# Kernel tuning notes

Hardware: AMD Instinct MI355X
Metric: run time of the kernel (lower is better)

## Reference

```python
import jax, jax.numpy as jnp
import numpy as np
from jax import lax

K = 3          # dcn kernel size
KK = K * K     # 9 taps
PAD = 1


def _conv(x, w, b, pad):
    y = lax.conv_general_dilated(
        x, w, window_strides=(1, 1), padding=[(pad, pad), (pad, pad)],
        dimension_numbers=("NCHW", "OIHW", "NCHW"))
    return y + b[None, :, None, None]


def _bilinear_gather(x, py, px):
    """Zero-padded bilinear sampling.
    x: [B,C,Hin,Win]; py,px: [B,KK,H,W] float sample coords.
    returns [B,C,KK,H,W]."""
    B, C, Hin, Win = x.shape
    y0 = jnp.floor(py)
    x0 = jnp.floor(px)
    ly = py - y0   # frac weights
    lx = px - x0
    xf = x.reshape(B, C, Hin * Win)

    def corner(yc, xc, w):
        valid = (yc >= 0) & (yc <= Hin - 1) & (xc >= 0) & (xc <= Win - 1)
        yi = jnp.clip(yc, 0, Hin - 1).astype(jnp.int32)
        xi = jnp.clip(xc, 0, Win - 1).astype(jnp.int32)
        idx = yi * Win + xi                              # [B,KK,H,W]
        vals = jax.vmap(lambda f, i: jnp.take(f, i, axis=1))(xf, idx)  # [B,C,KK,H,W]
        return vals * (w * valid.astype(x.dtype))[:, None]

    out = corner(y0,     x0,     (1 - ly) * (1 - lx))
    out = out + corner(y0,     x0 + 1, (1 - ly) * lx)
    out = out + corner(y0 + 1, x0,     ly * (1 - lx))
    out = out + corner(y0 + 1, x0 + 1, ly * lx)
    return out


def _forward(x, conv1_w, conv1_b, off_w, off_b, dcn_w, dcn_b):
    # features: Conv2d(1,3,3,s1,p1) + ReLU + MaxPool(3,2)
    h = jax.nn.relu(_conv(x, conv1_w, conv1_b, pad=1))
    h = lax.reduce_window(h, -jnp.inf, lax.max,
                          window_dimensions=(1, 1, 3, 3),
                          window_strides=(1, 1, 2, 2), padding="VALID")
    B, C, H, W = h.shape

    # DCNv2: conv_offset_mask -> (dy, dx, sigmoid mask)
    om = _conv(h, off_w, off_b, pad=PAD)          # [B, 3*KK, H, W]
    dy = om[:, :KK]
    dx = om[:, KK:2 * KK]
    mask = jax.nn.sigmoid(om[:, 2 * KK:])         # [B, KK, H, W]

    # base sampling grid (stride 1, pad 1, dilation 1)
    ky = (jnp.arange(KK) // K).astype(h.dtype)    # kernel row of each tap
    kx = (jnp.arange(KK) % K).astype(h.dtype)
    hh = jnp.arange(H, dtype=h.dtype)
    ww = jnp.arange(W, dtype=h.dtype)
    py = hh[None, None, :, None] - PAD + ky[None, :, None, None] + dy
    px = ww[None, None, None, :] - PAD + kx[None, :, None, None] + dx

    sampled = _bilinear_gather(h, py, px)          # [B,C,KK,H,W]
    sampled = sampled * mask[:, None]              # modulation
    out = jnp.einsum("bckhw,ock->bohw", sampled,
                     dcn_w.reshape(dcn_w.shape[0], C, KK))
    return out + dcn_b[None, :, None, None]


def setup_inputs() -> dict:
    key = jax.random.key(0)
    ks = jax.random.split(key, 7)
    x = jax.random.normal(ks[0], (32, 1, 512, 512), dtype=jnp.float32)
    conv1_w = jax.random.normal(ks[1], (3, 1, 3, 3), dtype=jnp.float32) * 0.5
    conv1_b = jnp.zeros((3,), dtype=jnp.float32)
    # offset/mask conv: 3*KK = 27 output channels; small init so offsets are modest
    off_w = jax.random.normal(ks[2], (3 * KK, 3, 3, 3), dtype=jnp.float32) * 0.01
    off_b = jax.random.normal(ks[3], (3 * KK,), dtype=jnp.float32) * 0.01
    dcn_w = jax.random.normal(ks[4], (3, 3, 3, 3), dtype=jnp.float32) * 0.1
    dcn_b = jnp.zeros((3,), dtype=jnp.float32)
    return {"x": x, "conv1_w": conv1_w, "conv1_b": conv1_b,
            "off_w": off_w, "off_b": off_b, "dcn_w": dcn_w, "dcn_b": dcn_b}


def reference(x, conv1_w, conv1_b, off_w, off_b, dcn_w, dcn_b):
    return _forward(x, conv1_w, conv1_b, off_w, off_b, dcn_w, dcn_b)
```

## Files before the change

kernel.cpp:

```cpp
#include <hip/hip_runtime.h>
#include <math.h>

#define B_  32
#define H0  512
#define W0  512
#define Hh  255
#define Wh  255
#define HP  259

typedef __attribute__((ext_vector_type(8))) short    bf16x8;
typedef __attribute__((ext_vector_type(4))) float    f32x4;
typedef __attribute__((ext_vector_type(4))) unsigned int u32x4;

static __device__ __forceinline__ unsigned int f2bf(float f) {
    unsigned int u = __float_as_uint(f);
    return (u + 0x7FFFu + ((u >> 16) & 1u)) >> 16;
}
static __device__ __forceinline__ float bflo(unsigned int u) { return __uint_as_float(u << 16); }
static __device__ __forceinline__ float bfhi(unsigned int u) { return __uint_as_float(u & 0xFFFF0000u); }

__global__ __launch_bounds__(256) void conv_pool_kernel(
    const float* __restrict__ x,
    const float* __restrict__ w,
    const float* __restrict__ bias,
    uint2* __restrict__ hp)
{
    const int b = blockIdx.z;
    const int tx = threadIdx.x, ty = threadIdx.y;
    const int tid = ty * 16 + tx;

    if (blockIdx.y == 16) {
        uint2* hpb = hp + b * (HP * HP);
        const int gid = blockIdx.x * 256 + tid;
        if (gid < 2072) {
            int r, c;
            if (gid < 1036) {
                int rr = gid / 259; c = gid - rr * 259;
                r = rr + (rr >= 2 ? 255 : 0);
            } else {
                int u = gid - 1036;
                int cc = u / 259; r = u - cc * 259;
                c = cc + (cc >= 2 ? 255 : 0);
            }
            hpb[r * HP + c] = make_uint2(0u, 0u);
        }
        return;
    }

    __shared__ float sx[35][36];
    __shared__ float sc[33 * 100];
    const int i0 = blockIdx.y * 16;
    const int j0 = blockIdx.x * 16;

    const float* xb = x + b * (H0 * W0);
    for (int t = tid; t < 35 * 35; t += 256) {
        int r = t / 35, c = t - r * 35;
        int gr = 2 * i0 - 1 + r;
        int gc = 2 * j0 - 1 + c;
        float v = 0.f;
        if ((unsigned)gr < (unsigned)H0 && (unsigned)gc < (unsigned)W0) v = xb[gr * W0 + gc];
        sx[r][c] = v;
    }
    __syncthreads();

    float w0[9], w1[9], w2[9];
#pragma unroll
    for (int t = 0; t < 9; ++t) { w0[t] = w[t]; w1[t] = w[9 + t]; w2[t] = w[18 + t]; }
    const float b0 = bias[0], b1 = bias[1], b2 = bias[2];

    for (int t = tid; t < 33 * 33; t += 256) {
        int r = t / 33, c = t - r * 33;
        float s0 = b0, s1 = b1, s2 = b2;
#pragma unroll
        for (int ky = 0; ky < 3; ++ky) {
#pragma unroll
            for (int kx = 0; kx < 3; ++kx) {
                float v = sx[r + ky][c + kx];
                s0 = fmaf(w0[ky * 3 + kx], v, s0);
                s1 = fmaf(w1[ky * 3 + kx], v, s1);
                s2 = fmaf(w2[ky * 3 + kx], v, s2);
            }
        }
        float* p = &sc[r * 100 + c * 3];
        p[0] = s0; p[1] = s1; p[2] = s2;
    }
    __syncthreads();

    const int i = i0 + ty, j = j0 + tx;
    if (i >= Hh || j >= Wh) return;

    const float* r0 = &sc[(2 * ty + 0) * 100 + (2 * tx) * 3];
    const float* r1 = &sc[(2 * ty + 1) * 100 + (2 * tx) * 3];
    const float* r2 = &sc[(2 * ty + 2) * 100 + (2 * tx) * 3];
#define MAX3_(a, bq, cq) fmaxf(fmaxf((a), (bq)), (cq))
    float m0 = MAX3_(MAX3_(r0[0], r0[3], r0[6]), MAX3_(r1[0], r1[3], r1[6]), MAX3_(r2[0], r2[3], r2[6]));
    float m1 = MAX3_(MAX3_(r0[1], r0[4], r0[7]), MAX3_(r1[1], r1[4], r1[7]), MAX3_(r2[1], r2[4], r2[7]));
    float m2 = MAX3_(MAX3_(r0[2], r0[5], r0[8]), MAX3_(r1[2], r1[5], r1[8]), MAX3_(r2[2], r2[5], r2[8]));
    m0 = fmaxf(m0, 0.f); m1 = fmaxf(m1, 0.f); m2 = fmaxf(m2, 0.f);

    uint2 v;
    v.x = f2bf(m0) | (f2bf(m1) << 16);
    v.y = f2bf(m2);
    hp[(b * HP + i + 2) * HP + (j + 2)] = v;
}

__global__ __launch_bounds__(256, 5) void dcn_kernel(
    const uint2* __restrict__ hp,
    const float* __restrict__ off_w,
    const float* __restrict__ off_b,
    const float* __restrict__ dcn_w,
    const float* __restrict__ dcn_b,
    float* __restrict__ out)
{
    __shared__ __align__(16) char smem[18432];

    const int y   = blockIdx.x;
    const int b   = blockIdx.y;
    const int tid = threadIdx.x;
    const int x   = tid;

    const uint2* hb = hp + b * (HP * HP);

    {
        unsigned short* Bm = (unsigned short*)(smem + 16384);
        for (int idx = tid; idx < 1024; idx += 256) {
            int n = idx >> 5, k = idx & 31;
            float v = 0.f;
            if (n < 27) { if (k < 27) v = off_w[n * 27 + k]; else if (k == 27) v = off_b[n]; }
            Bm[n * 32 + k] = (unsigned short)f2bf(v);
        }
    }

    unsigned int L[9], Hv[9];
#pragma unroll
    for (int ky = 0; ky < 3; ++ky) {
        const unsigned int rbase = (unsigned int)(y + 1 + ky) * HP + (unsigned int)(x + 1);
#pragma unroll
        for (int kx = 0; kx < 3; ++kx) {
            uint2 v = hb[rbase + kx];
            L[ky * 3 + kx]  = v.x;
            Hv[ky * 3 + kx] = v.y;
        }
    }

    {
        unsigned int T[16];
        T[0]  = (L[0] & 0xFFFFu) | (L[1] << 16);
        T[1]  = (L[2] & 0xFFFFu) | (L[3] << 16);
        T[2]  = (L[4] & 0xFFFFu) | (L[5] << 16);
        T[3]  = (L[6] & 0xFFFFu) | (L[7] << 16);
        T[4]  = (L[8] & 0xFFFFu) | (L[0] & 0xFFFF0000u);
        T[5]  = (L[1] >> 16) | (L[2] & 0xFFFF0000u);
        T[6]  = (L[3] >> 16) | (L[4] & 0xFFFF0000u);
        T[7]  = (L[5] >> 16) | (L[6] & 0xFFFF0000u);
        T[8]  = (L[7] >> 16) | (L[8] & 0xFFFF0000u);
        T[9]  = (Hv[0] & 0xFFFFu) | (Hv[1] << 16);
        T[10] = (Hv[2] & 0xFFFFu) | (Hv[3] << 16);
        T[11] = (Hv[4] & 0xFFFFu) | (Hv[5] << 16);
        T[12] = (Hv[6] & 0xFFFFu) | (Hv[7] << 16);
        T[13] = (Hv[8] & 0xFFFFu) | 0x3F800000u;
        T[14] = 0u;
        T[15] = 0u;
#pragma unroll
        for (int c4 = 0; c4 < 4; ++c4) {
            u32x4 v = { T[c4 * 4 + 0], T[c4 * 4 + 1], T[c4 * 4 + 2], T[c4 * 4 + 3] };
            *(u32x4*)(smem + (c4 * 256 + tid) * 16) = v;
        }
    }
    __syncthreads();

    {
        const int wave = tid >> 6, lane = tid & 63;
        const int lrow = lane & 15, lchunk = lane >> 4;
        const short* As = (const short*)smem;
        const short* Bs = (const short*)(smem + 16384);

        bf16x8 afr[4];
#pragma unroll
        for (int m = 0; m < 4; ++m)
            afr[m] = *(const bf16x8*)(As + (lchunk * 256 + wave * 64 + m * 16 + lrow) * 8);
        bf16x8 bfr[2];
#pragma unroll
        for (int nt = 0; nt < 2; ++nt)
            bfr[nt] = *(const bf16x8*)(Bs + ((nt * 16 + lrow) * 32 + lchunk * 8));

        f32x4 acc[4][2];
#pragma unroll
        for (int m = 0; m < 4; ++m)
#pragma unroll
            for (int nt = 0; nt < 2; ++nt) {
                f32x4 z = {0.f, 0.f, 0.f, 0.f};
                acc[m][nt] = __builtin_amdgcn_mfma_f32_16x16x32_bf16(bfr[nt], afr[m], z, 0, 0, 0);
            }
        __syncthreads();

#pragma unroll
        for (int m = 0; m < 4; ++m)
#pragma unroll
            for (int nt = 0; nt < 2; ++nt) {
                const int n0  = nt * 16 + lchunk * 4;
                const int pxw = wave * 64 + m * 16 + lrow;
                unsigned int p0 = (__float_as_uint(acc[m][nt][0]) >> 16) |
                                  (__float_as_uint(acc[m][nt][1]) & 0xFFFF0000u);
                unsigned int p1 = (__float_as_uint(acc[m][nt][2]) >> 16) |
                                  (__float_as_uint(acc[m][nt][3]) & 0xFFFF0000u);
                unsigned int* q = (unsigned int*)(smem + pxw * 68 + n0 * 2);
                q[0] = p0;
                q[1] = p1;
            }
    }
    __syncthreads();

    unsigned int o2[14];
    {
        const unsigned int* omp = (const unsigned int*)(smem + x * 68);
#pragma unroll
        for (int j = 0; j < 14; ++j) o2[j] = omp[j];
    }
#define OM_(n) (((n) & 1) ? bfhi(o2[(n) >> 1]) : bflo(o2[(n) >> 1]))

    float outv0 = dcn_b[0], outv1 = dcn_b[1], outv2 = dcn_b[2];
    const float yf = (float)y, xf = (float)x;

#pragma unroll
    for (int k = 0; k < 9; ++k) {
        const float dy  = OM_(k);
        const float dxx = OM_(9 + k);
        const float zm  = OM_(18 + k);
        const float msk = __builtin_amdgcn_rcpf(1.f + __expf(-zm));

        const float py = yf + (float)(k / 3 - 1) + dy;
        const float px = xf + (float)(k % 3 - 1) + dxx;

        const float y0f = floorf(py), x0f = floorf(px);
        const float ly = py - y0f, lx = px - x0f;
        int iy = (int)y0f + 2, ix = (int)x0f + 2;
        iy = min(max(iy, 0), 257);
        ix = min(max(ix, 0), 257);

        const unsigned int idx = (unsigned int)iy * HP + (unsigned int)ix;
        u32x4 ua, ub;
        __builtin_memcpy(&ua, hb + idx, 16);
        __builtin_memcpy(&ub, hb + idx + HP, 16);

        const float my1 = ly * msk;
        const float my0 = msk - my1;
        const float lx1 = 1.f - lx;
        const float w00 = my0 * lx1, w01 = my0 * lx;
        const float w10 = my1 * lx1, w11 = my1 * lx;

        const float s0 = w00 * bflo(ua.x) + w01 * bflo(ua.z) + w10 * bflo(ub.x) + w11 * bflo(ub.z);
        const float s1 = w00 * bfhi(ua.x) + w01 * bfhi(ua.z) + w10 * bfhi(ub.x) + w11 * bfhi(ub.z);
        const float s2 = w00 * bflo(ua.y) + w01 * bflo(ua.w) + w10 * bflo(ub.y) + w11 * bflo(ub.w);

        outv0 = fmaf(dcn_w[0 * 27 + 0 * 9 + k], s0, outv0);
        outv0 = fmaf(dcn_w[0 * 27 + 1 * 9 + k], s1, outv0);
        outv0 = fmaf(dcn_w[0 * 27 + 2 * 9 + k], s2, outv0);
        outv1 = fmaf(dcn_w[1 * 27 + 0 * 9 + k], s0, outv1);
        outv1 = fmaf(dcn_w[1 * 27 + 1 * 9 + k], s1, outv1);
        outv1 = fmaf(dcn_w[1 * 27 + 2 * 9 + k], s2, outv1);
        outv2 = fmaf(dcn_w[2 * 27 + 0 * 9 + k], s0, outv2);
        outv2 = fmaf(dcn_w[2 * 27 + 1 * 9 + k], s1, outv2);
        outv2 = fmaf(dcn_w[2 * 27 + 2 * 9 + k], s2, outv2);
    }

    if (x < Wh) {
        const int hwsz = Hh * Wh;
        const int o = (b * 3) * hwsz + y * Wh + x;
        out[o]            = outv0;
        out[o + hwsz]     = outv1;
        out[o + 2 * hwsz] = outv2;
    }
}

extern "C" void kernel_launch(void* const* d_in, const int* in_sizes, int n_in,
                              void* d_out, int out_size, void* d_ws, size_t ws_size,
                              hipStream_t stream) {
    const float* x       = (const float*)d_in[0];
    const float* conv1_w = (const float*)d_in[1];
    const float* conv1_b = (const float*)d_in[2];
    const float* off_w   = (const float*)d_in[3];
    const float* off_b   = (const float*)d_in[4];
    const float* dcn_w   = (const float*)d_in[5];
    const float* dcn_b   = (const float*)d_in[6];
    float* out = (float*)d_out;
    uint2* hp  = (uint2*)d_ws;

    conv_pool_kernel<<<dim3(16, 17, B_), dim3(16, 16), 0, stream>>>(x, conv1_w, conv1_b, hp);
    dcn_kernel<<<dim3(Hh, B_), 256, 0, stream>>>(hp, off_w, off_b, dcn_w, dcn_b, out);
}
```

Baseline: 69.87 us.

## Switch intermediate storage and MFMA from bf16 to fp16 with packed half2 bilinear math

The pooled feature map and offset-conv weights are now stored as fp16 instead of bf16, and the offset MFMA uses the f16 variant. The bilinear corner blend becomes packed half2 FMAs instead of scalar fp32 FMAs with bf16 unpacking. The 3x3 neighbourhood load is also widened to one 16-byte load plus one 8-byte load per row. This aims to cut VALU instruction count in the gather loop, at the cost of lower accumulation precision in fp16 and possible overflow or accuracy risk.

```diff
diff --git a/kernel.cpp b/kernel.cpp
--- a/kernel.cpp
+++ b/kernel.cpp
@@ -1,4 +1,5 @@
 #include <hip/hip_runtime.h>
+#include <hip/hip_fp16.h>
 #include <math.h>
 
 #define B_  32
@@ -8,16 +9,16 @@
 #define Wh  255
 #define HP  259
 
-typedef __attribute__((ext_vector_type(8))) short    bf16x8;
+typedef __attribute__((ext_vector_type(8))) _Float16 f16x8;
 typedef __attribute__((ext_vector_type(4))) float    f32x4;
 typedef __attribute__((ext_vector_type(4))) unsigned int u32x4;
 
-static __device__ __forceinline__ unsigned int f2bf(float f) {
-    unsigned int u = __float_as_uint(f);
-    return (u + 0x7FFFu + ((u >> 16) & 1u)) >> 16;
-}
-static __device__ __forceinline__ float bflo(unsigned int u) { return __uint_as_float(u << 16); }
-static __device__ __forceinline__ float bfhi(unsigned int u) { return __uint_as_float(u & 0xFFFF0000u); }
+static __device__ __forceinline__ __half2 u2h2(unsigned int u) {
+    __half2 h; __builtin_memcpy(&h, &u, 4); return h;
+}
+static __device__ __forceinline__ unsigned int h2u(__half2 h) {
+    unsigned int u; __builtin_memcpy(&u, &h, 4); return u;
+}
 
 __global__ __launch_bounds__(256) void conv_pool_kernel(
     const float* __restrict__ x,
@@ -99,8 +100,8 @@
     m0 = fmaxf(m0, 0.f); m1 = fmaxf(m1, 0.f); m2 = fmaxf(m2, 0.f);
 
     uint2 v;
-    v.x = f2bf(m0) | (f2bf(m1) << 16);
-    v.y = f2bf(m2);
+    v.x = h2u(__floats2half2_rn(m0, m1));
+    v.y = (unsigned int)__half_as_ushort(__float2half_rn(m2));
     hp[(b * HP + i + 2) * HP + (j + 2)] = v;
 }
 
@@ -127,7 +128,7 @@
             int n = idx >> 5, k = idx & 31;
             float v = 0.f;
             if (n < 27) { if (k < 27) v = off_w[n * 27 + k]; else if (k == 27) v = off_b[n]; }
-            Bm[n * 32 + k] = (unsigned short)f2bf(v);
+            Bm[n * 32 + k] = __half_as_ushort(__float2half_rn(v));
         }
     }
 
@@ -135,12 +136,12 @@
 #pragma unroll
     for (int ky = 0; ky < 3; ++ky) {
         const unsigned int rbase = (unsigned int)(y + 1 + ky) * HP + (unsigned int)(x + 1);
-#pragma unroll
-        for (int kx = 0; kx < 3; ++kx) {
-            uint2 v = hb[rbase + kx];
-            L[ky * 3 + kx]  = v.x;
-            Hv[ky * 3 + kx] = v.y;
-        }
+        u32x4 r01;
+        __builtin_memcpy(&r01, hb + rbase, 16);
+        uint2 r2 = hb[rbase + 2];
+        L[ky * 3 + 0]  = r01.x;  Hv[ky * 3 + 0] = r01.y;
+        L[ky * 3 + 1]  = r01.z;  Hv[ky * 3 + 1] = r01.w;
+        L[ky * 3 + 2]  = r2.x;   Hv[ky * 3 + 2] = r2.y;
     }
 
     {
@@ -158,7 +159,7 @@
         T[10] = (Hv[2] & 0xFFFFu) | (Hv[3] << 16);
         T[11] = (Hv[4] & 0xFFFFu) | (Hv[5] << 16);
         T[12] = (Hv[6] & 0xFFFFu) | (Hv[7] << 16);
-        T[13] = (Hv[8] & 0xFFFFu) | 0x3F800000u;
+        T[13] = (Hv[8] & 0xFFFFu) | 0x3C000000u;
         T[14] = 0u;
         T[15] = 0u;
 #pragma unroll
@@ -172,17 +173,17 @@
     {
         const int wave = tid >> 6, lane = tid & 63;
         const int lrow = lane & 15, lchunk = lane >> 4;
-        const short* As = (const short*)smem;
-        const short* Bs = (const short*)(smem + 16384);
-
-        bf16x8 afr[4];
+        const _Float16* As = (const _Float16*)smem;
+        const _Float16* Bs = (const _Float16*)(smem + 16384);
+
+        f16x8 afr[4];
 #pragma unroll
         for (int m = 0; m < 4; ++m)
-            afr[m] = *(const bf16x8*)(As + (lchunk * 256 + wave * 64 + m * 16 + lrow) * 8);
-        bf16x8 bfr[2];
+            afr[m] = *(const f16x8*)(As + (lchunk * 256 + wave * 64 + m * 16 + lrow) * 8);
+        f16x8 bfr[2];
 #pragma unroll
         for (int nt = 0; nt < 2; ++nt)
-            bfr[nt] = *(const bf16x8*)(Bs + ((nt * 16 + lrow) * 32 + lchunk * 8));
+            bfr[nt] = *(const f16x8*)(Bs + ((nt * 16 + lrow) * 32 + lchunk * 8));
 
         f32x4 acc[4][2];
 #pragma unroll
@@ -190,7 +191,7 @@
 #pragma unroll
             for (int nt = 0; nt < 2; ++nt) {
                 f32x4 z = {0.f, 0.f, 0.f, 0.f};
-                acc[m][nt] = __builtin_amdgcn_mfma_f32_16x16x32_bf16(bfr[nt], afr[m], z, 0, 0, 0);
+                acc[m][nt] = __builtin_amdgcn_mfma_f32_16x16x32_f16(bfr[nt], afr[m], z, 0, 0, 0);
             }
         __syncthreads();
 
@@ -200,10 +201,8 @@
             for (int nt = 0; nt < 2; ++nt) {
                 const int n0  = nt * 16 + lchunk * 4;
                 const int pxw = wave * 64 + m * 16 + lrow;
-                unsigned int p0 = (__float_as_uint(acc[m][nt][0]) >> 16) |
-                                  (__float_as_uint(acc[m][nt][1]) & 0xFFFF0000u);
-                unsigned int p1 = (__float_as_uint(acc[m][nt][2]) >> 16) |
-                                  (__float_as_uint(acc[m][nt][3]) & 0xFFFF0000u);
+                unsigned int p0 = h2u(__floats2half2_rn(acc[m][nt][0], acc[m][nt][1]));
+                unsigned int p1 = h2u(__floats2half2_rn(acc[m][nt][2], acc[m][nt][3]));
                 unsigned int* q = (unsigned int*)(smem + pxw * 68 + n0 * 2);
                 q[0] = p0;
                 q[1] = p1;
@@ -217,7 +216,7 @@
 #pragma unroll
         for (int j = 0; j < 14; ++j) o2[j] = omp[j];
     }
-#define OM_(n) (((n) & 1) ? bfhi(o2[(n) >> 1]) : bflo(o2[(n) >> 1]))
+#define OM_(n) (((n) & 1) ? __high2float(u2h2(o2[(n) >> 1])) : __low2float(u2h2(o2[(n) >> 1])))
 
     float outv0 = dcn_b[0], outv1 = dcn_b[1], outv2 = dcn_b[2];
     const float yf = (float)y, xf = (float)x;
@@ -249,9 +248,21 @@
         const float w00 = my0 * lx1, w01 = my0 * lx;
         const float w10 = my1 * lx1, w11 = my1 * lx;
 
-        const float s0 = w00 * bflo(ua.x) + w01 * bflo(ua.z) + w10 * bflo(ub.x) + w11 * bflo(ub.z);
-        const float s1 = w00 * bfhi(ua.x) + w01 * bfhi(ua.z) + w10 * bfhi(ub.x) + w11 * bfhi(ub.z);
-        const float s2 = w00 * bflo(ua.y) + w01 * bflo(ua.w) + w10 * bflo(ub.y) + w11 * bflo(ub.w);
+        const __half2 W00 = __float2half2_rn(w00);
+        const __half2 W01 = __float2half2_rn(w01);
+        const __half2 W10 = __float2half2_rn(w10);
+        const __half2 W11 = __float2half2_rn(w11);
+        __half2 sA = __hmul2(W00, u2h2(ua.x));
+        sA = __hfma2(W01, u2h2(ua.z), sA);
+        sA = __hfma2(W10, u2h2(ub.x), sA);
+        sA = __hfma2(W11, u2h2(ub.z), sA);
+        __half2 sB = __hmul2(W00, u2h2(ua.y));
+        sB = __hfma2(W01, u2h2(ua.w), sB);
+        sB = __hfma2(W10, u2h2(ub.y), sB);
+        sB = __hfma2(W11, u2h2(ub.w), sB);
+        const float s0 = __low2float(sA);
+        const float s1 = __high2float(sA);
+        const float s2 = __low2float(sB);
 
         outv0 = fmaf(dcn_w[0 * 27 + 0 * 9 + k], s0, outv0);
         outv0 = fmaf(dcn_w[0 * 27 + 1 * 9 + k], s1, outv0);
```

Result: faster. 67.17 us (-3.9%).
